# Kernel optimization log

Measured on AMD Instinct MI355X. Metric: run time of the kernel, lower is better.

The kernel has to match this reference:

```python
import jax, jax.numpy as jnp
import numpy as np

B, L, E, H, Dff = 2, 2048, 1024, 16, 4096
Dh = E // H


def _ln(x, g, b, eps=1e-5):
    m = jnp.mean(x, axis=-1, keepdims=True)
    v = jnp.mean((x - m) ** 2, axis=-1, keepdims=True)
    return (x - m) / jnp.sqrt(v + eps) * g + b


def setup_inputs() -> dict:
    key = jax.random.key(0)
    ks = jax.random.split(key, 16)
    s_e = 1.0 / np.sqrt(E)
    s_d = 1.0 / np.sqrt(Dff)
    inp = {
        "x": jax.random.normal(ks[0], (B, L, E), jnp.float32),
        # causal mask: positions with 0 are masked out (masked_fill(mask==0, -1e9))
        "mask": jnp.tril(jnp.ones((L, L), jnp.bool_)),
        # per-head QKV projections, stacked over heads: (H, E, Dh), biases (H, Dh)
        "Wq": jax.random.uniform(ks[1], (H, E, Dh), jnp.float32, -s_e, s_e),
        "bq": jax.random.uniform(ks[2], (H, Dh), jnp.float32, -s_e, s_e),
        "Wk": jax.random.uniform(ks[3], (H, E, Dh), jnp.float32, -s_e, s_e),
        "bk": jax.random.uniform(ks[4], (H, Dh), jnp.float32, -s_e, s_e),
        "Wv": jax.random.uniform(ks[5], (H, E, Dh), jnp.float32, -s_e, s_e),
        "bv": jax.random.uniform(ks[6], (H, Dh), jnp.float32, -s_e, s_e),
        "Wo": jax.random.uniform(ks[7], (E, E), jnp.float32, -s_e, s_e),
        "bo": jax.random.uniform(ks[8], (E,), jnp.float32, -s_e, s_e),
        "W1": jax.random.uniform(ks[9], (E, Dff), jnp.float32, -s_e, s_e),
        "c1": jax.random.uniform(ks[10], (Dff,), jnp.float32, -s_e, s_e),
        "W2": jax.random.uniform(ks[11], (Dff, E), jnp.float32, -s_d, s_d),
        "c2": jax.random.uniform(ks[12], (E,), jnp.float32, -s_d, s_d),
        "g1": jnp.ones((E,), jnp.float32),
        "beta1": jnp.zeros((E,), jnp.float32),
        "g2": jnp.ones((E,), jnp.float32),
        "beta2": jnp.zeros((E,), jnp.float32),
    }
    return inp


def reference(x, mask, Wq, bq, Wk, bk, Wv, bv, Wo, bo, W1, c1, W2, c2, g1, beta1, g2, beta2):
    # Batched equivalent of the per-head Attention loop (eval mode: dropout = identity)
    q = jnp.einsum("ble,hed->bhld", x, Wq) + bq[None, :, None, :]
    k = jnp.einsum("ble,hed->bhld", x, Wk) + bk[None, :, None, :]
    v = jnp.einsum("ble,hed->bhld", x, Wv) + bv[None, :, None, :]
    scores = jnp.einsum("bhld,bhmd->bhlm", q, k) / np.sqrt(Dh).astype(np.float32)
    scores = jnp.where(mask[None, None, :, :], scores, -1e9)
    p = jax.nn.softmax(scores, axis=-1)
    z = jnp.einsum("bhlm,bhmd->bhld", p, v)  # (B,H,L,Dh)
    z = z.transpose(0, 2, 1, 3).reshape(B, L, E)  # concat heads
    att = z @ Wo + bo
    h = _ln(x + att, g1, beta1)
    ff = jax.nn.relu(h @ W1 + c1) @ W2 + c2
    out = _ln(h + ff, g2, beta2)
    return out
```

## Files before the change

kernel.cpp:

```cpp
#include <hip/hip_runtime.h>
#include <hip/hip_bf16.h>
#include <math.h>

#define B_   2
#define L_   2048
#define E_   1024
#define H_   16
#define DH   64
#define DFF  4096
#define M_   4096
#define APAD 72
#define SCALE_Q 0.18033688011112042f

typedef __attribute__((ext_vector_type(8))) short short8;
typedef __attribute__((ext_vector_type(4))) float f32x4;
typedef __bf16 bf16x8 __attribute__((ext_vector_type(8)));

__device__ __forceinline__ float bf2f(unsigned short u) {
    return __uint_as_float(((unsigned)u) << 16);
}
__device__ __forceinline__ unsigned short f2bf(float f) {
    unsigned u = __float_as_uint(f);
    return (unsigned short)((u + 0x7fff + ((u >> 16) & 1)) >> 16);
}
__device__ __forceinline__ unsigned pk_trunc(float lo, float hi) {
    return (__float_as_uint(lo) >> 16) | (__float_as_uint(hi) & 0xffff0000u);
}

__device__ __forceinline__ void gld16(const unsigned short* g, unsigned short* l) {
    __builtin_amdgcn_global_load_lds(
        (const __attribute__((address_space(1))) void*)g,
        (__attribute__((address_space(3))) void*)l, 16, 0, 0);
}

__global__ __launch_bounds__(256) void prep(const float* __restrict__ x,
                                            const float* __restrict__ Wq,
                                            const float* __restrict__ Wk,
                                            const float* __restrict__ Wv,
                                            const float* __restrict__ bq,
                                            const float* __restrict__ bk,
                                            const float* __restrict__ bv,
                                            const float* __restrict__ Wo,
                                            const float* __restrict__ W1,
                                            const float* __restrict__ W2,
                                            unsigned short* __restrict__ xb,
                                            unsigned short* __restrict__ Wqkvt,
                                            unsigned short* __restrict__ Wot,
                                            unsigned short* __restrict__ W1t,
                                            unsigned short* __restrict__ W2t,
                                            float* __restrict__ bqkv) {
    __shared__ float tile[32][33];
    int bid = blockIdx.x;
    const int t = threadIdx.x;

    if (bid < 4096) {
        int i = (bid * 256 + t) * 4;
        float4 v = *(const float4*)&x[i];
        ushort4 pk = { f2bf(v.x), f2bf(v.y), f2bf(v.z), f2bf(v.w) };
        *(ushort4*)&xb[i] = pk;
        return;
    }
    bid -= 4096;

    const float* in; unsigned short* outp; int R, C, r0, c0; float sc = 1.f;
    if (bid < 3072) {
        int xq = bid & 1, yq = (bid >> 1) & 31, wh = bid >> 6;
        int which = wh >> 4, h = wh & 15;
        in   = (which == 0 ? Wq : which == 1 ? Wk : Wv) + (size_t)h * E_ * DH;
        outp = Wqkvt + ((size_t)which * 1024 + h * 64) * 1024;
        R = E_; C = DH; r0 = yq * 32; c0 = xq * 32;
        if (which == 0) sc = SCALE_Q;
    } else if (bid < 4096) {
        bid -= 3072;
        in = Wo; outp = Wot; R = E_; C = E_;
        c0 = (bid & 31) * 32; r0 = (bid >> 5) * 32;
    } else if (bid < 8192) {
        bid -= 4096;
        in = W1; outp = W1t; R = E_; C = DFF;
        c0 = (bid & 127) * 32; r0 = (bid >> 7) * 32;
    } else if (bid < 12288) {
        bid -= 8192;
        in = W2; outp = W2t; R = DFF; C = E_;
        c0 = (bid & 31) * 32; r0 = (bid >> 5) * 32;
    } else {
        bid -= 12288;
        int n = bid * 256 + t;
        bqkv[n] = n < 1024 ? bq[n] * SCALE_Q : n < 2048 ? bk[n - 1024] : bv[n - 2048];
        return;
    }

    const int tx = t & 31, tq = t >> 5;
#pragma unroll
    for (int s2 = 0; s2 < 4; s2++)
        tile[tq * 4 + s2][tx] = in[(size_t)(r0 + tq * 4 + s2) * C + c0 + tx] * sc;
    __syncthreads();
#pragma unroll
    for (int s2 = 0; s2 < 4; s2++)
        outp[(size_t)(c0 + tq * 4 + s2) * R + r0 + tx] = f2bf(tile[tx][tq * 4 + s2]);
}

__global__ __launch_bounds__(256) void v_transpose_perm(const unsigned short* __restrict__ qkv,
                                                        unsigned short* __restrict__ vtg) {
    __shared__ unsigned short tile[64 * APAD];
    const int t  = threadIdx.x;
    const int kt = blockIdx.x, hh = blockIdx.y, b = blockIdx.z;
    const int rr0 = t >> 3, o8 = (t & 7) * 8, rr1 = rr0 + 32;
    const size_t gbase = ((size_t)b * L_ + kt * 64) * 3072 + 2048 + hh * 64;
    *(short8*)&tile[rr0 * APAD + o8] = *(const short8*)&qkv[gbase + (size_t)rr0 * 3072 + o8];
    *(short8*)&tile[rr1 * APAD + o8] = *(const short8*)&qkv[gbase + (size_t)rr1 * 3072 + o8];
    __syncthreads();
    const size_t obase = ((size_t)(b * H_ + hh) * 64) * (size_t)L_ + kt * 64;
    const int a = t & 15, d0 = (t >> 4) * 4;
#pragma unroll
    for (int s2 = 0; s2 < 4; s2++) {
        int d = d0 + s2;
        ushort4 pk = { tile[(a +  0) * APAD + d], tile[(a + 16) * APAD + d],
                       tile[(a + 32) * APAD + d], tile[(a + 48) * APAD + d] };
        *(ushort4*)&vtg[obase + (size_t)d * L_ + 4 * a] = pk;
    }
}

#define BAR() __builtin_amdgcn_s_barrier()
#define LGKM0() do { asm volatile("s_waitcnt lgkmcnt(0)" ::: "memory"); \
                     __builtin_amdgcn_sched_barrier(0); } while (0)

#define G256_READ_A(qr) do {                                                  \
    _Pragma("unroll") for (int mi = 0; mi < 4; mi++)                          \
    _Pragma("unroll") for (int ks = 0; ks < 2; ks++)                          \
        afr[mi][ks] = *(const bf16x8*)&As[bb + ((qr) * 128 + aRow + mi * 16) * 64 + (ks ? cs1 : cs0)]; \
} while (0)

#define G256_READ_B(qc) do {                                                  \
    _Pragma("unroll") for (int nj = 0; nj < 2; nj++)                          \
    _Pragma("unroll") for (int ks = 0; ks < 2; ks++)                          \
        bfr[qc][nj][ks] = *(const bf16x8*)&Bs[bb + ((qc) * 128 + bRow + nj * 16) * 64 + (ks ? cs1 : cs0)]; \
} while (0)

#define G256_MFMA(qr, qc) do {                                                \
    __builtin_amdgcn_s_setprio(1);                                            \
    _Pragma("unroll") for (int mi = 0; mi < 4; mi++)                          \
    _Pragma("unroll") for (int nj = 0; nj < 2; nj++)                          \
    _Pragma("unroll") for (int ks = 0; ks < 2; ks++)                          \
        acc[qr][qc][mi][nj] = __builtin_amdgcn_mfma_f32_16x16x32_bf16(        \
            afr[mi][ks], bfr[qc][nj][ks], acc[qr][qc][mi][nj], 0, 0, 0);      \
    __builtin_amdgcn_s_setprio(0);                                            \
} while (0)

template <int RELU, int SK>
__global__ __launch_bounds__(512, 2) void gemm256(const unsigned short* __restrict__ A,
                                                  const unsigned short* __restrict__ Bt,
                                                  const float* __restrict__ bias,
                                                  unsigned short* __restrict__ P0,
                                                  unsigned short* __restrict__ P1,
                                                  unsigned short* __restrict__ P2,
                                                  unsigned short* __restrict__ P3,
                                                  int M, int N, int K) {
    extern __shared__ __align__(16) unsigned short g_lds[];
    unsigned short* As = g_lds;
    unsigned short* Bs = g_lds + 32768;

    const int t    = threadIdx.x;
    const int lane = t & 63;
    const int w    = t >> 6;
    const int quad = lane >> 4;
    const int l16  = lane & 15;

    const int lin = blockIdx.x;
    const int xcd = lin & 7, s = lin >> 3;
    const int m0 = ((xcd << 1) | (s & 1)) * 256;
    const int rest = s >> 1;
    int n0, kbeg, KT;
    unsigned short* C;
    if (SK) {
        n0 = (rest & 3) * 256;
        const int z  = rest >> 2;
        const int K4 = K >> 2;
        kbeg = z * K4;
        KT   = K4 >> 6;
        C = (z == 0) ? P0 : (z == 1) ? P1 : (z == 2) ? P2 : P3;
    } else {
        n0 = rest * 256;
        kbeg = 0;
        KT   = K >> 6;
        C = P0;
    }

    const int srow = t >> 3;
    const int ksw  = ((t & 7) ^ (srow & 7)) * 8;
    const size_t aStage = (size_t)(m0 + srow) * K + kbeg + ksw;
    const size_t bStage = (size_t)(n0 + srow) * K + kbeg + ksw;

    auto stageA = [&](int buf, int h, int v) {
        size_t g = aStage + (size_t)(h * 128) * K + (size_t)v * 64;
        unsigned short* l = As + buf * 16384 + h * 8192 + w * 512;
        gld16(A + g, l);
        gld16(A + g + (size_t)64 * K, l + 4096);
    };
    auto stageB = [&](int buf, int h, int v) {
        size_t g = bStage + (size_t)(h * 128) * K + (size_t)v * 64;
        unsigned short* l = Bs + buf * 16384 + h * 8192 + w * 512;
        gld16(Bt + g, l);
        gld16(Bt + g + (size_t)64 * K, l + 4096);
    };

    const int aRow = (w >> 2) * 64 + l16;
    const int bRow = (w & 3) * 32 + l16;
    const int cs0  = (quad ^ (l16 & 7)) * 8;
    const int cs1  = cs0 ^ 32;

    f32x4 acc[2][2][4][2];
#pragma unroll
    for (int a1 = 0; a1 < 2; a1++)
#pragma unroll
        for (int a2 = 0; a2 < 2; a2++)
#pragma unroll
            for (int a3 = 0; a3 < 4; a3++)
#pragma unroll
                for (int a4 = 0; a4 < 2; a4++)
                    acc[a1][a2][a3][a4] = (f32x4){0.f, 0.f, 0.f, 0.f};

    bf16x8 afr[4][2], bfr[2][2][2];

    stageA(0, 0, 0); stageA(0, 1, 0); stageB(0, 0, 0); stageB(0, 1, 0);
    if (KT > 1) {
        stageA(1, 0, 1); stageB(1, 0, 1);
        asm volatile("s_waitcnt vmcnt(4)" ::: "memory");
    } else {
        asm volatile("s_waitcnt vmcnt(0)" ::: "memory");
    }
    BAR();

    for (int u = 0; u < KT; ++u) {
        const int bb = (u & 1) * 16384;
        const int nb = ((u + 1) & 1);

        G256_READ_A(0);
        G256_READ_B(0);
        if (u + 1 < KT) stageB(nb, 1, u + 1);
        BAR(); LGKM0();
        G256_MFMA(0, 0);
        BAR();

        G256_READ_B(1);
        if (u + 1 < KT) stageA(nb, 1, u + 1);
        BAR(); LGKM0();
        G256_MFMA(0, 1);
        BAR();

        G256_READ_A(1);
        if (u + 2 < KT) stageA(u & 1, 0, u + 2);
        BAR(); LGKM0();
        G256_MFMA(1, 0);
        BAR();

        if (u + 2 < KT) {
            stageB(u & 1, 0, u + 2);
            asm volatile("s_waitcnt vmcnt(4)" ::: "memory");
        } else {
            asm volatile("s_waitcnt vmcnt(0)" ::: "memory");
        }
        BAR(); LGKM0();
        G256_MFMA(1, 1);
        BAR();
    }

#pragma unroll
    for (int qr = 0; qr < 2; qr++)
#pragma unroll
        for (int qc = 0; qc < 2; qc++)
#pragma unroll
            for (int nj = 0; nj < 2; nj++) {
                const int col = n0 + qc * 128 + (w & 3) * 32 + nj * 16 + l16;
                const float bv = SK ? 0.f : bias[col];
#pragma unroll
                for (int mi = 0; mi < 4; mi++) {
                    const int row = m0 + qr * 128 + (w >> 2) * 64 + mi * 16 + quad * 4;
#pragma unroll
                    for (int r = 0; r < 4; r++) {
                        float v = acc[qr][qc][mi][nj][r] + bv;
                        if (RELU) v = fmaxf(v, 0.f);
                        C[(size_t)(row + r) * N + col] = f2bf(v);
                    }
                }
            }
}

__global__ __launch_bounds__(256, 3) void attn_mfma(const unsigned short* __restrict__ qkv,
                                                    const unsigned short* __restrict__ vtg,
                                                    unsigned short* __restrict__ zb) {
    __shared__ __align__(16) unsigned short ks[2][64 * APAD];
    __shared__ __align__(16) unsigned short vt[64 * APAD];
    __shared__ __align__(16) unsigned short ps[128 * APAD];

    const int t    = threadIdx.x;
    const int lane = t & 63;
    const int w    = t >> 6;
    const int l16  = lane & 15;
    const int quad = lane >> 4;

    const int lin  = blockIdx.x;
    const int xcd  = lin & 7;
    const int s    = lin >> 3;
    const int hh   = xcd * 2 + (s & 1);
    const int rest = s >> 1;
    const int b    = rest & 1;
    const int qq0  = rest >> 1;
    const int qq   = b ? qq0 : 15 - qq0;

    const size_t rowbase = (size_t)b * L_;
    const size_t vbase   = ((size_t)(b * H_ + hh) * 64) * (size_t)L_;

    bf16x8 qf[2][2];
#pragma unroll
    for (int g = 0; g < 2; g++) {
        size_t qrow = rowbase + qq * 128 + w * 32 + g * 16 + l16;
#pragma unroll
        for (int c = 0; c < 2; c++)
            qf[g][c] = *(const bf16x8*)&qkv[qrow * 3072 + hh * 64 + c * 32 + quad * 8];
    }

    f32x4 o[2][4];
#pragma unroll
    for (int g = 0; g < 2; g++)
#pragma unroll
        for (int j = 0; j < 4; j++) o[g][j] = (f32x4){0.f, 0.f, 0.f, 0.f};
    float l_i[2][4] = {};

    const int rr0 = t >> 3, o8 = (t & 7) * 8, rr1 = rr0 + 32;
    const int ktmax = 2 * qq + 1;

    {
        size_t kg = rowbase * 3072 + 1024 + hh * 64;
        short8 k0 = *(const short8*)&qkv[kg + (size_t)rr0 * 3072 + o8];
        short8 k1 = *(const short8*)&qkv[kg + (size_t)rr1 * 3072 + o8];
        short8 v0 = *(const short8*)&vtg[vbase + (size_t)rr0 * L_ + o8];
        short8 v1 = *(const short8*)&vtg[vbase + (size_t)rr1 * L_ + o8];
        *(short8*)&ks[0][rr0 * APAD + o8] = k0;
        *(short8*)&ks[0][rr1 * APAD + o8] = k1;
        *(short8*)&vt[rr0 * APAD + o8] = v0;
        *(short8*)&vt[rr1 * APAD + o8] = v1;
    }

    short8 kr0, kr1, vr0, vr1;
    for (int kt = 0; kt <= ktmax; kt++) {
        const int p = kt & 1;
        __syncthreads();

        if (kt < ktmax) {
            size_t kg = (rowbase + (kt + 1) * 64) * 3072 + 1024 + hh * 64;
            kr0 = *(const short8*)&qkv[kg + (size_t)rr0 * 3072 + o8];
            kr1 = *(const short8*)&qkv[kg + (size_t)rr1 * 3072 + o8];
            size_t vg = vbase + (kt + 1) * 64;
            vr0 = *(const short8*)&vtg[vg + (size_t)rr0 * L_ + o8];
            vr1 = *(const short8*)&vtg[vg + (size_t)rr1 * L_ + o8];
        }

        f32x4 s4[2][4];
#pragma unroll
        for (int g = 0; g < 2; g++)
#pragma unroll
            for (int j = 0; j < 4; j++) s4[g][j] = (f32x4){0.f, 0.f, 0.f, 0.f};
#pragma unroll
        for (int c = 0; c < 2; c++)
#pragma unroll
            for (int j = 0; j < 4; j++) {
                bf16x8 kf = *(const bf16x8*)&ks[p][(j * 16 + l16) * APAD + c * 32 + quad * 8];
#pragma unroll
                for (int g = 0; g < 2; g++)
                    s4[g][j] = __builtin_amdgcn_mfma_f32_16x16x32_bf16(qf[g][c], kf, s4[g][j], 0, 0, 0);
            }

        if (kt >= 2 * qq) {
#pragma unroll
            for (int g = 0; g < 2; g++)
#pragma unroll
                for (int j = 0; j < 4; j++) {
                    int lk = kt * 64 + j * 16 + l16;
#pragma unroll
                    for (int r = 0; r < 4; r++)
                        if (lk > qq * 128 + w * 32 + g * 16 + quad * 4 + r)
                            s4[g][j][r] = -INFINITY;
                }
        }

#pragma unroll
        for (int g = 0; g < 2; g++)
#pragma unroll
            for (int r = 0; r < 4; r++) {
                float p0 = __builtin_amdgcn_exp2f(s4[g][0][r]);
                float p1 = __builtin_amdgcn_exp2f(s4[g][1][r]);
                float p2 = __builtin_amdgcn_exp2f(s4[g][2][r]);
                float p3 = __builtin_amdgcn_exp2f(s4[g][3][r]);
                l_i[g][r] += (p0 + p1) + (p2 + p3);
                uint2 pk = { pk_trunc(p0, p1), pk_trunc(p2, p3) };
                *(uint2*)&ps[(w * 32 + g * 16 + quad * 4 + r) * APAD + 4 * l16] = pk;
            }

        __builtin_amdgcn_s_waitcnt(0xc07f);

#pragma unroll
        for (int c = 0; c < 2; c++) {
            bf16x8 pf[2];
#pragma unroll
            for (int g = 0; g < 2; g++)
                pf[g] = *(const bf16x8*)&ps[(w * 32 + g * 16 + l16) * APAD + c * 32 + quad * 8];
#pragma unroll
            for (int j = 0; j < 4; j++) {
                bf16x8 vf = *(const bf16x8*)&vt[(j * 16 + l16) * APAD + c * 32 + quad * 8];
#pragma unroll
                for (int g = 0; g < 2; g++)
                    o[g][j] = __builtin_amdgcn_mfma_f32_16x16x32_bf16(pf[g], vf, o[g][j], 0, 0, 0);
            }
        }

        __syncthreads();
        if (kt < ktmax) {
            *(short8*)&ks[p ^ 1][rr0 * APAD + o8] = kr0;
            *(short8*)&ks[p ^ 1][rr1 * APAD + o8] = kr1;
            *(short8*)&vt[rr0 * APAD + o8] = vr0;
            *(short8*)&vt[rr1 * APAD + o8] = vr1;
        }
    }

#pragma unroll
    for (int g = 0; g < 2; g++)
#pragma unroll
        for (int r = 0; r < 4; r++) {
            float l = l_i[g][r];
            l += __shfl_xor(l, 1);
            l += __shfl_xor(l, 2);
            l += __shfl_xor(l, 4);
            l += __shfl_xor(l, 8);
            float inv = 1.f / l;
            size_t row = rowbase + qq * 128 + w * 32 + g * 16 + quad * 4 + r;
#pragma unroll
            for (int j = 0; j < 4; j++)
                zb[row * 1024 + hh * 64 + j * 16 + l16] = f2bf(o[g][j][r] * inv);
        }
}

template <int WRITE_BF16>
__global__ __launch_bounds__(256) void ln5_kernel(const float* __restrict__ a,
                                                  const unsigned short* __restrict__ q0,
                                                  const unsigned short* __restrict__ q1,
                                                  const unsigned short* __restrict__ q2,
                                                  const unsigned short* __restrict__ q3,
                                                  const float* __restrict__ bias,
                                                  const float* __restrict__ g,
                                                  const float* __restrict__ be,
                                                  float* __restrict__ out,
                                                  unsigned short* __restrict__ out_bf) {
    __shared__ float s1[256], s2[256];
    const int row = blockIdx.x;
    const int t   = threadIdx.x;
    const size_t base = (size_t)row * E_ + t * 4;

    float4 ya = *(const float4*)&a[base];
    ushort4 u0 = *(const ushort4*)&q0[base];
    ushort4 u1 = *(const ushort4*)&q1[base];
    ushort4 u2 = *(const ushort4*)&q2[base];
    ushort4 u3 = *(const ushort4*)&q3[base];
    float4 bb = *(const float4*)&bias[t * 4];
    float y0 = ya.x + bb.x + bf2f(u0.x) + bf2f(u1.x) + bf2f(u2.x) + bf2f(u3.x);
    float y1 = ya.y + bb.y + bf2f(u0.y) + bf2f(u1.y) + bf2f(u2.y) + bf2f(u3.y);
    float y2 = ya.z + bb.z + bf2f(u0.z) + bf2f(u1.z) + bf2f(u2.z) + bf2f(u3.z);
    float y3 = ya.w + bb.w + bf2f(u0.w) + bf2f(u1.w) + bf2f(u2.w) + bf2f(u3.w);

    s1[t] = y0 + y1 + y2 + y3;
    s2[t] = y0 * y0 + y1 * y1 + y2 * y2 + y3 * y3;
    __syncthreads();
    for (int off = 128; off > 0; off >>= 1) {
        if (t < off) { s1[t] += s1[t + off]; s2[t] += s2[t + off]; }
        __syncthreads();
    }
    float mean = s1[0] * (1.0f / E_);
    float var  = s2[0] * (1.0f / E_) - mean * mean;
    float rstd = rsqrtf(var + 1e-5f);

    float4 gv = *(const float4*)&g[t * 4];
    float4 bv = *(const float4*)&be[t * 4];
    float4 ov;
    ov.x = (y0 - mean) * rstd * gv.x + bv.x;
    ov.y = (y1 - mean) * rstd * gv.y + bv.y;
    ov.z = (y2 - mean) * rstd * gv.z + bv.z;
    ov.w = (y3 - mean) * rstd * gv.w + bv.w;
    *(float4*)&out[base] = ov;
    if (WRITE_BF16) {
        ushort4 pk = { f2bf(ov.x), f2bf(ov.y), f2bf(ov.z), f2bf(ov.w) };
        *(ushort4*)&out_bf[base] = pk;
    }
}

extern "C" void kernel_launch(void* const* d_in, const int* in_sizes, int n_in,
                              void* d_out, int out_size, void* d_ws, size_t ws_size,
                              hipStream_t stream)
{
    const float* x     = (const float*)d_in[0];
    const float* Wq    = (const float*)d_in[2];
    const float* bq    = (const float*)d_in[3];
    const float* Wk    = (const float*)d_in[4];
    const float* bk    = (const float*)d_in[5];
    const float* Wv    = (const float*)d_in[6];
    const float* bv    = (const float*)d_in[7];
    const float* Wo    = (const float*)d_in[8];
    const float* bo    = (const float*)d_in[9];
    const float* W1    = (const float*)d_in[10];
    const float* c1    = (const float*)d_in[11];
    const float* W2    = (const float*)d_in[12];
    const float* c2    = (const float*)d_in[13];
    const float* g1    = (const float*)d_in[14];
    const float* beta1 = (const float*)d_in[15];
    const float* g2    = (const float*)d_in[16];
    const float* beta2 = (const float*)d_in[17];
    float* out = (float*)d_out;

    const size_t MB = 1024 * 1024;
    char* w = (char*)d_ws;
    unsigned short* xb    = (unsigned short*)(w + 0 * MB);
    unsigned short* Wqkvt = (unsigned short*)(w + 8 * MB);
    unsigned short* Wot   = (unsigned short*)(w + 14 * MB);
    unsigned short* W1t   = (unsigned short*)(w + 16 * MB);
    unsigned short* W2t   = (unsigned short*)(w + 24 * MB);
    float*          bqkv  = (float*)(w + 32 * MB);
    unsigned short* qkv   = (unsigned short*)(w + 33 * MB);
    unsigned short* zb    = (unsigned short*)(w + 57 * MB);
    float*          h     = (float*)(w + 65 * MB);
    unsigned short* vtg   = (unsigned short*)(w + 89 * MB);
    unsigned short* ap0   = (unsigned short*)(w + 33 * MB);
    unsigned short* ap1   = (unsigned short*)(w + 41 * MB);
    unsigned short* ap2   = (unsigned short*)(w + 49 * MB);
    unsigned short* ap3   = (unsigned short*)(w + 89 * MB);
    unsigned short* hb    = (unsigned short*)(w + 0 * MB);
    unsigned short* ff1b  = (unsigned short*)(w + 33 * MB);
    unsigned short* fp0   = (unsigned short*)(w + 0 * MB);
    unsigned short* fp1   = (unsigned short*)(w + 8 * MB);
    unsigned short* fp2   = (unsigned short*)(w + 16 * MB);
    unsigned short* fp3   = (unsigned short*)(w + 81 * MB);

    static bool lds_inited = false;
    if (!lds_inited) {
        (void)hipFuncSetAttribute((const void*)&gemm256<0, 0>,
                                  hipFuncAttributeMaxDynamicSharedMemorySize, 131072);
        (void)hipFuncSetAttribute((const void*)&gemm256<1, 0>,
                                  hipFuncAttributeMaxDynamicSharedMemorySize, 131072);
        (void)hipFuncSetAttribute((const void*)&gemm256<0, 1>,
                                  hipFuncAttributeMaxDynamicSharedMemorySize, 131072);
        lds_inited = true;
    }

    dim3 blk(256);
    dim3 blk2(512);

    prep<<<dim3(16396), blk, 0, stream>>>(x, Wq, Wk, Wv, bq, bk, bv, Wo, W1, W2,
                                          xb, Wqkvt, Wot, W1t, W2t, bqkv);

    gemm256<0, 0><<<dim3(192), blk2, 131072, stream>>>(xb, Wqkvt, bqkv,
                                                       qkv, nullptr, nullptr, nullptr,
                                                       M_, 3072, E_);

    v_transpose_perm<<<dim3(L_ / 64, H_, B_), blk, 0, stream>>>(qkv, vtg);

    attn_mfma<<<dim3(512), blk, 0, stream>>>(qkv, vtg, zb);

    gemm256<0, 1><<<dim3(256), blk2, 131072, stream>>>(zb, Wot, nullptr,
                                                       ap0, ap1, ap2, ap3,
                                                       M_, E_, E_);

    ln5_kernel<1><<<dim3(M_), blk, 0, stream>>>(x, ap0, ap1, ap2, ap3, bo, g1, beta1, h, hb);

    gemm256<1, 0><<<dim3(256), blk2, 131072, stream>>>(hb, W1t, c1,
                                                       ff1b, nullptr, nullptr, nullptr,
                                                       M_, DFF, E_);

    gemm256<0, 1><<<dim3(256), blk2, 131072, stream>>>(ff1b, W2t, nullptr,
                                                       fp0, fp1, fp2, fp3,
                                                       M_, E_, DFF);

    ln5_kernel<0><<<dim3(M_), blk, 0, stream>>>(h, fp0, fp1, fp2, fp3, c2, g2, beta2, out, nullptr);
}
```

Baseline: 341.3 us.

## Split attention work across 8 waves with 16 query rows each

The attention kernel now launches 512 threads per block, and each of 8 waves owns 16 query rows instead of 4 waves owning 32 rows each. Per-wave register state (Q fragments, accumulators, row sums) is halved, and each thread loads one K and one V chunk per tile instead of two. The aim is more resident waves and better latency hiding. In exchange, each K/V fragment read from LDS is reused for half as many MFMAs, so LDS traffic per FLOP doubles, and block-wide barriers now have to synchronize twice as many waves.

```diff
diff --git a/kernel.cpp b/kernel.cpp
--- a/kernel.cpp
+++ b/kernel.cpp
@@ -285,7 +285,7 @@
             }
 }
 
-__global__ __launch_bounds__(256, 3) void attn_mfma(const unsigned short* __restrict__ qkv,
+__global__ __launch_bounds__(512, 4) void attn_mfma(const unsigned short* __restrict__ qkv,
                                                     const unsigned short* __restrict__ vtg,
                                                     unsigned short* __restrict__ zb) {
     __shared__ __align__(16) unsigned short ks[2][64 * APAD];
@@ -310,133 +310,106 @@
     const size_t rowbase = (size_t)b * L_;
     const size_t vbase   = ((size_t)(b * H_ + hh) * 64) * (size_t)L_;
 
-    bf16x8 qf[2][2];
-#pragma unroll
-    for (int g = 0; g < 2; g++) {
-        size_t qrow = rowbase + qq * 128 + w * 32 + g * 16 + l16;
+    bf16x8 qf[2];
+    {
+        size_t qrow = rowbase + qq * 128 + w * 16 + l16;
 #pragma unroll
         for (int c = 0; c < 2; c++)
-            qf[g][c] = *(const bf16x8*)&qkv[qrow * 3072 + hh * 64 + c * 32 + quad * 8];
-    }
-
-    f32x4 o[2][4];
-#pragma unroll
-    for (int g = 0; g < 2; g++)
-#pragma unroll
-        for (int j = 0; j < 4; j++) o[g][j] = (f32x4){0.f, 0.f, 0.f, 0.f};
-    float l_i[2][4] = {};
-
-    const int rr0 = t >> 3, o8 = (t & 7) * 8, rr1 = rr0 + 32;
+            qf[c] = *(const bf16x8*)&qkv[qrow * 3072 + hh * 64 + c * 32 + quad * 8];
+    }
+
+    f32x4 o[4];
+#pragma unroll
+    for (int j = 0; j < 4; j++) o[j] = (f32x4){0.f, 0.f, 0.f, 0.f};
+    float l_i[4] = {};
+
+    const int rr = t >> 3, o8 = (t & 7) * 8;
     const int ktmax = 2 * qq + 1;
 
     {
         size_t kg = rowbase * 3072 + 1024 + hh * 64;
-        short8 k0 = *(const short8*)&qkv[kg + (size_t)rr0 * 3072 + o8];
-        short8 k1 = *(const short8*)&qkv[kg + (size_t)rr1 * 3072 + o8];
-        short8 v0 = *(const short8*)&vtg[vbase + (size_t)rr0 * L_ + o8];
-        short8 v1 = *(const short8*)&vtg[vbase + (size_t)rr1 * L_ + o8];
-        *(short8*)&ks[0][rr0 * APAD + o8] = k0;
-        *(short8*)&ks[0][rr1 * APAD + o8] = k1;
-        *(short8*)&vt[rr0 * APAD + o8] = v0;
-        *(short8*)&vt[rr1 * APAD + o8] = v1;
-    }
-
-    short8 kr0, kr1, vr0, vr1;
+        short8 k0 = *(const short8*)&qkv[kg + (size_t)rr * 3072 + o8];
+        short8 v0 = *(const short8*)&vtg[vbase + (size_t)rr * L_ + o8];
+        *(short8*)&ks[0][rr * APAD + o8] = k0;
+        *(short8*)&vt[rr * APAD + o8] = v0;
+    }
+
+    short8 kr0, vr0;
     for (int kt = 0; kt <= ktmax; kt++) {
         const int p = kt & 1;
         __syncthreads();
 
         if (kt < ktmax) {
             size_t kg = (rowbase + (kt + 1) * 64) * 3072 + 1024 + hh * 64;
-            kr0 = *(const short8*)&qkv[kg + (size_t)rr0 * 3072 + o8];
-            kr1 = *(const short8*)&qkv[kg + (size_t)rr1 * 3072 + o8];
-            size_t vg = vbase + (kt + 1) * 64;
-            vr0 = *(const short8*)&vtg[vg + (size_t)rr0 * L_ + o8];
-            vr1 = *(const short8*)&vtg[vg + (size_t)rr1 * L_ + o8];
+            kr0 = *(const short8*)&qkv[kg + (size_t)rr * 3072 + o8];
+            vr0 = *(const short8*)&vtg[vbase + (kt + 1) * 64 + (size_t)rr * L_ + o8];
         }
 
-        f32x4 s4[2][4];
-#pragma unroll
-        for (int g = 0; g < 2; g++)
-#pragma unroll
-            for (int j = 0; j < 4; j++) s4[g][j] = (f32x4){0.f, 0.f, 0.f, 0.f};
+        f32x4 s4[4];
+#pragma unroll
+        for (int j = 0; j < 4; j++) s4[j] = (f32x4){0.f, 0.f, 0.f, 0.f};
 #pragma unroll
         for (int c = 0; c < 2; c++)
 #pragma unroll
             for (int j = 0; j < 4; j++) {
                 bf16x8 kf = *(const bf16x8*)&ks[p][(j * 16 + l16) * APAD + c * 32 + quad * 8];
-#pragma unroll
-                for (int g = 0; g < 2; g++)
-                    s4[g][j] = __builtin_amdgcn_mfma_f32_16x16x32_bf16(qf[g][c], kf, s4[g][j], 0, 0, 0);
+                s4[j] = __builtin_amdgcn_mfma_f32_16x16x32_bf16(qf[c], kf, s4[j], 0, 0, 0);
             }
 
         if (kt >= 2 * qq) {
 #pragma unroll
-            for (int g = 0; g < 2; g++)
-#pragma unroll
-                for (int j = 0; j < 4; j++) {
-                    int lk = kt * 64 + j * 16 + l16;
-#pragma unroll
-                    for (int r = 0; r < 4; r++)
-                        if (lk > qq * 128 + w * 32 + g * 16 + quad * 4 + r)
-                            s4[g][j][r] = -INFINITY;
-                }
+            for (int j = 0; j < 4; j++) {
+                int lk = kt * 64 + j * 16 + l16;
+#pragma unroll
+                for (int r = 0; r < 4; r++)
+                    if (lk > qq * 128 + w * 16 + quad * 4 + r)
+                        s4[j][r] = -INFINITY;
+            }
         }
 
 #pragma unroll
-        for (int g = 0; g < 2; g++)
-#pragma unroll
-            for (int r = 0; r < 4; r++) {
-                float p0 = __builtin_amdgcn_exp2f(s4[g][0][r]);
-                float p1 = __builtin_amdgcn_exp2f(s4[g][1][r]);
-                float p2 = __builtin_amdgcn_exp2f(s4[g][2][r]);
-                float p3 = __builtin_amdgcn_exp2f(s4[g][3][r]);
-                l_i[g][r] += (p0 + p1) + (p2 + p3);
-                uint2 pk = { pk_trunc(p0, p1), pk_trunc(p2, p3) };
-                *(uint2*)&ps[(w * 32 + g * 16 + quad * 4 + r) * APAD + 4 * l16] = pk;
-            }
+        for (int r = 0; r < 4; r++) {
+            float p0 = __builtin_amdgcn_exp2f(s4[0][r]);
+            float p1 = __builtin_amdgcn_exp2f(s4[1][r]);
+            float p2 = __builtin_amdgcn_exp2f(s4[2][r]);
+            float p3 = __builtin_amdgcn_exp2f(s4[3][r]);
+            l_i[r] += (p0 + p1) + (p2 + p3);
+            uint2 pk = { pk_trunc(p0, p1), pk_trunc(p2, p3) };
+            *(uint2*)&ps[(w * 16 + quad * 4 + r) * APAD + 4 * l16] = pk;
+        }
 
         __builtin_amdgcn_s_waitcnt(0xc07f);
 
 #pragma unroll
         for (int c = 0; c < 2; c++) {
-            bf16x8 pf[2];
-#pragma unroll
-            for (int g = 0; g < 2; g++)
-                pf[g] = *(const bf16x8*)&ps[(w * 32 + g * 16 + l16) * APAD + c * 32 + quad * 8];
+            bf16x8 pf = *(const bf16x8*)&ps[(w * 16 + l16) * APAD + c * 32 + quad * 8];
 #pragma unroll
             for (int j = 0; j < 4; j++) {
                 bf16x8 vf = *(const bf16x8*)&vt[(j * 16 + l16) * APAD + c * 32 + quad * 8];
-#pragma unroll
-                for (int g = 0; g < 2; g++)
-                    o[g][j] = __builtin_amdgcn_mfma_f32_16x16x32_bf16(pf[g], vf, o[g][j], 0, 0, 0);
+                o[j] = __builtin_amdgcn_mfma_f32_16x16x32_bf16(pf, vf, o[j], 0, 0, 0);
             }
         }
 
         __syncthreads();
         if (kt < ktmax) {
-            *(short8*)&ks[p ^ 1][rr0 * APAD + o8] = kr0;
-            *(short8*)&ks[p ^ 1][rr1 * APAD + o8] = kr1;
-            *(short8*)&vt[rr0 * APAD + o8] = vr0;
-            *(short8*)&vt[rr1 * APAD + o8] = vr1;
+            *(short8*)&ks[p ^ 1][rr * APAD + o8] = kr0;
+            *(short8*)&vt[rr * APAD + o8] = vr0;
         }
     }
 
 #pragma unroll
-    for (int g = 0; g < 2; g++)
-#pragma unroll
-        for (int r = 0; r < 4; r++) {
-            float l = l_i[g][r];
-            l += __shfl_xor(l, 1);
-            l += __shfl_xor(l, 2);
-            l += __shfl_xor(l, 4);
-            l += __shfl_xor(l, 8);
-            float inv = 1.f / l;
-            size_t row = rowbase + qq * 128 + w * 32 + g * 16 + quad * 4 + r;
-#pragma unroll
-            for (int j = 0; j < 4; j++)
-                zb[row * 1024 + hh * 64 + j * 16 + l16] = f2bf(o[g][j][r] * inv);
-        }
+    for (int r = 0; r < 4; r++) {
+        float l = l_i[r];
+        l += __shfl_xor(l, 1);
+        l += __shfl_xor(l, 2);
+        l += __shfl_xor(l, 4);
+        l += __shfl_xor(l, 8);
+        float inv = 1.f / l;
+        size_t row = rowbase + qq * 128 + w * 16 + quad * 4 + r;
+#pragma unroll
+        for (int j = 0; j < 4; j++)
+            zb[row * 1024 + hh * 64 + j * 16 + l16] = f2bf(o[j][r] * inv);
+    }
 }
 
 template <int WRITE_BF16>
@@ -560,7 +533,7 @@
 
     v_transpose_perm<<<dim3(L_ / 64, H_, B_), blk, 0, stream>>>(qkv, vtg);
 
-    attn_mfma<<<dim3(512), blk, 0, stream>>>(qkv, vtg, zb);
+    attn_mfma<<<dim3(512), blk2, 0, stream>>>(qkv, vtg, zb);
 
     gemm256<0, 1><<<dim3(256), blk2, 131072, stream>>>(zb, Wot, nullptr,
                                                        ap0, ap1, ap2, ap3,
```

Result: no change. 338.2 us (-0.9%).

## Split attention KV range across two blocks with paired q-tiles and combine pass

Applied to the files above, without the earlier changes.

Each attention block now processes a pair of query tiles (qq and 15-qq) and only even or odd KV tiles, based on a new unit index. This balances causal work across blocks. Partial fp32 outputs and row sums go to workspace, and a new attn_combine kernel sums the halves, normalises and writes bf16 z. The MFMA sections also gain s_setprio hints and launch bounds drop to 2 blocks per CU. In exchange, the extra kernel launch and the fp32 partial traffic add cost.

```diff
diff --git a/kernel.cpp b/kernel.cpp
--- a/kernel.cpp
+++ b/kernel.cpp
@@ -285,9 +285,12 @@
             }
 }
 
-__global__ __launch_bounds__(256, 3) void attn_mfma(const unsigned short* __restrict__ qkv,
+__global__ __launch_bounds__(256, 2) void attn_mfma(const unsigned short* __restrict__ qkv,
                                                     const unsigned short* __restrict__ vtg,
-                                                    unsigned short* __restrict__ zb) {
+                                                    float* __restrict__ oA,
+                                                    float* __restrict__ oB,
+                                                    float* __restrict__ lA,
+                                                    float* __restrict__ lB) {
     __shared__ __align__(16) unsigned short ks[2][64 * APAD];
     __shared__ __align__(16) unsigned short vt[64 * APAD];
     __shared__ __align__(16) unsigned short ps[128 * APAD];
@@ -299,144 +302,180 @@
     const int quad = lane >> 4;
 
     const int lin  = blockIdx.x;
-    const int xcd  = lin & 7;
-    const int s    = lin >> 3;
+    const int unit = lin >> 8;
+    const int l8   = lin & 255;
+    const int xcd  = l8 & 7;
+    const int s    = l8 >> 3;
     const int hh   = xcd * 2 + (s & 1);
     const int rest = s >> 1;
     const int b    = rest & 1;
-    const int qq0  = rest >> 1;
-    const int qq   = b ? qq0 : 15 - qq0;
+    const int pair = rest >> 1;
+
+    float* __restrict__ oP = unit ? oB : oA;
+    float* __restrict__ lP = unit ? lB : lA;
 
     const size_t rowbase = (size_t)b * L_;
     const size_t vbase   = ((size_t)(b * H_ + hh) * 64) * (size_t)L_;
-
-    bf16x8 qf[2][2];
-#pragma unroll
-    for (int g = 0; g < 2; g++) {
-        size_t qrow = rowbase + qq * 128 + w * 32 + g * 16 + l16;
-#pragma unroll
-        for (int c = 0; c < 2; c++)
-            qf[g][c] = *(const bf16x8*)&qkv[qrow * 3072 + hh * 64 + c * 32 + quad * 8];
-    }
-
-    f32x4 o[2][4];
-#pragma unroll
-    for (int g = 0; g < 2; g++)
-#pragma unroll
-        for (int j = 0; j < 4; j++) o[g][j] = (f32x4){0.f, 0.f, 0.f, 0.f};
-    float l_i[2][4] = {};
-
     const int rr0 = t >> 3, o8 = (t & 7) * 8, rr1 = rr0 + 32;
-    const int ktmax = 2 * qq + 1;
-
-    {
-        size_t kg = rowbase * 3072 + 1024 + hh * 64;
-        short8 k0 = *(const short8*)&qkv[kg + (size_t)rr0 * 3072 + o8];
-        short8 k1 = *(const short8*)&qkv[kg + (size_t)rr1 * 3072 + o8];
-        short8 v0 = *(const short8*)&vtg[vbase + (size_t)rr0 * L_ + o8];
-        short8 v1 = *(const short8*)&vtg[vbase + (size_t)rr1 * L_ + o8];
-        *(short8*)&ks[0][rr0 * APAD + o8] = k0;
-        *(short8*)&ks[0][rr1 * APAD + o8] = k1;
-        *(short8*)&vt[rr0 * APAD + o8] = v0;
-        *(short8*)&vt[rr1 * APAD + o8] = v1;
-    }
-
-    short8 kr0, kr1, vr0, vr1;
-    for (int kt = 0; kt <= ktmax; kt++) {
-        const int p = kt & 1;
-        __syncthreads();
-
-        if (kt < ktmax) {
-            size_t kg = (rowbase + (kt + 1) * 64) * 3072 + 1024 + hh * 64;
-            kr0 = *(const short8*)&qkv[kg + (size_t)rr0 * 3072 + o8];
-            kr1 = *(const short8*)&qkv[kg + (size_t)rr1 * 3072 + o8];
-            size_t vg = vbase + (kt + 1) * 64;
-            vr0 = *(const short8*)&vtg[vg + (size_t)rr0 * L_ + o8];
-            vr1 = *(const short8*)&vtg[vg + (size_t)rr1 * L_ + o8];
+
+    for (int ph = 0; ph < 2; ph++) {
+        const int qq = ph ? pair : 15 - pair;
+        const int cnt = qq + 1;
+
+        bf16x8 qf[2][2];
+#pragma unroll
+        for (int g = 0; g < 2; g++) {
+            size_t qrow = rowbase + qq * 128 + w * 32 + g * 16 + l16;
+#pragma unroll
+            for (int c = 0; c < 2; c++)
+                qf[g][c] = *(const bf16x8*)&qkv[qrow * 3072 + hh * 64 + c * 32 + quad * 8];
         }
 
-        f32x4 s4[2][4];
+        f32x4 o[2][4];
 #pragma unroll
         for (int g = 0; g < 2; g++)
 #pragma unroll
-            for (int j = 0; j < 4; j++) s4[g][j] = (f32x4){0.f, 0.f, 0.f, 0.f};
-#pragma unroll
-        for (int c = 0; c < 2; c++)
-#pragma unroll
-            for (int j = 0; j < 4; j++) {
-                bf16x8 kf = *(const bf16x8*)&ks[p][(j * 16 + l16) * APAD + c * 32 + quad * 8];
+            for (int j = 0; j < 4; j++) o[g][j] = (f32x4){0.f, 0.f, 0.f, 0.f};
+        float l_i[2][4] = {};
+
+        {
+            size_t kg = (rowbase + unit * 64) * 3072 + 1024 + hh * 64;
+            short8 k0 = *(const short8*)&qkv[kg + (size_t)rr0 * 3072 + o8];
+            short8 k1 = *(const short8*)&qkv[kg + (size_t)rr1 * 3072 + o8];
+            short8 v0 = *(const short8*)&vtg[vbase + unit * 64 + (size_t)rr0 * L_ + o8];
+            short8 v1 = *(const short8*)&vtg[vbase + unit * 64 + (size_t)rr1 * L_ + o8];
+            *(short8*)&ks[0][rr0 * APAD + o8] = k0;
+            *(short8*)&ks[0][rr1 * APAD + o8] = k1;
+            *(short8*)&vt[rr0 * APAD + o8] = v0;
+            *(short8*)&vt[rr1 * APAD + o8] = v1;
+        }
+
+        short8 kr0, kr1, vr0, vr1;
+        for (int i = 0; i < cnt; i++) {
+            const int kt = unit + 2 * i;
+            const int p  = i & 1;
+            __syncthreads();
+
+            if (i + 1 < cnt) {
+                size_t kg = (rowbase + (kt + 2) * 64) * 3072 + 1024 + hh * 64;
+                kr0 = *(const short8*)&qkv[kg + (size_t)rr0 * 3072 + o8];
+                kr1 = *(const short8*)&qkv[kg + (size_t)rr1 * 3072 + o8];
+                size_t vg = vbase + (kt + 2) * 64;
+                vr0 = *(const short8*)&vtg[vg + (size_t)rr0 * L_ + o8];
+                vr1 = *(const short8*)&vtg[vg + (size_t)rr1 * L_ + o8];
+            }
+
+            f32x4 s4[2][4];
+#pragma unroll
+            for (int g = 0; g < 2; g++)
+#pragma unroll
+                for (int j = 0; j < 4; j++) s4[g][j] = (f32x4){0.f, 0.f, 0.f, 0.f};
+            __builtin_amdgcn_s_setprio(1);
+#pragma unroll
+            for (int c = 0; c < 2; c++)
+#pragma unroll
+                for (int j = 0; j < 4; j++) {
+                    bf16x8 kf = *(const bf16x8*)&ks[p][(j * 16 + l16) * APAD + c * 32 + quad * 8];
+#pragma unroll
+                    for (int g = 0; g < 2; g++)
+                        s4[g][j] = __builtin_amdgcn_mfma_f32_16x16x32_bf16(qf[g][c], kf, s4[g][j], 0, 0, 0);
+                }
+            __builtin_amdgcn_s_setprio(0);
+
+            if (kt >= 2 * qq) {
 #pragma unroll
                 for (int g = 0; g < 2; g++)
-                    s4[g][j] = __builtin_amdgcn_mfma_f32_16x16x32_bf16(qf[g][c], kf, s4[g][j], 0, 0, 0);
+#pragma unroll
+                    for (int j = 0; j < 4; j++) {
+                        int lk = kt * 64 + j * 16 + l16;
+#pragma unroll
+                        for (int r = 0; r < 4; r++)
+                            if (lk > qq * 128 + w * 32 + g * 16 + quad * 4 + r)
+                                s4[g][j][r] = -INFINITY;
+                    }
             }
 
-        if (kt >= 2 * qq) {
 #pragma unroll
             for (int g = 0; g < 2; g++)
 #pragma unroll
+                for (int r = 0; r < 4; r++) {
+                    float p0 = __builtin_amdgcn_exp2f(s4[g][0][r]);
+                    float p1 = __builtin_amdgcn_exp2f(s4[g][1][r]);
+                    float p2 = __builtin_amdgcn_exp2f(s4[g][2][r]);
+                    float p3 = __builtin_amdgcn_exp2f(s4[g][3][r]);
+                    l_i[g][r] += (p0 + p1) + (p2 + p3);
+                    uint2 pk = { pk_trunc(p0, p1), pk_trunc(p2, p3) };
+                    *(uint2*)&ps[(w * 32 + g * 16 + quad * 4 + r) * APAD + 4 * l16] = pk;
+                }
+
+            __builtin_amdgcn_s_waitcnt(0xc07f);
+
+            __builtin_amdgcn_s_setprio(1);
+#pragma unroll
+            for (int c = 0; c < 2; c++) {
+                bf16x8 pf[2];
+#pragma unroll
+                for (int g = 0; g < 2; g++)
+                    pf[g] = *(const bf16x8*)&ps[(w * 32 + g * 16 + l16) * APAD + c * 32 + quad * 8];
+#pragma unroll
                 for (int j = 0; j < 4; j++) {
-                    int lk = kt * 64 + j * 16 + l16;
-#pragma unroll
-                    for (int r = 0; r < 4; r++)
-                        if (lk > qq * 128 + w * 32 + g * 16 + quad * 4 + r)
-                            s4[g][j][r] = -INFINITY;
+                    bf16x8 vf = *(const bf16x8*)&vt[(j * 16 + l16) * APAD + c * 32 + quad * 8];
+#pragma unroll
+                    for (int g = 0; g < 2; g++)
+                        o[g][j] = __builtin_amdgcn_mfma_f32_16x16x32_bf16(pf[g], vf, o[g][j], 0, 0, 0);
                 }
-        }
-
-#pragma unroll
-        for (int g = 0; g < 2; g++)
-#pragma unroll
-            for (int r = 0; r < 4; r++) {
-                float p0 = __builtin_amdgcn_exp2f(s4[g][0][r]);
-                float p1 = __builtin_amdgcn_exp2f(s4[g][1][r]);
-                float p2 = __builtin_amdgcn_exp2f(s4[g][2][r]);
-                float p3 = __builtin_amdgcn_exp2f(s4[g][3][r]);
-                l_i[g][r] += (p0 + p1) + (p2 + p3);
-                uint2 pk = { pk_trunc(p0, p1), pk_trunc(p2, p3) };
-                *(uint2*)&ps[(w * 32 + g * 16 + quad * 4 + r) * APAD + 4 * l16] = pk;
             }
-
-        __builtin_amdgcn_s_waitcnt(0xc07f);
-
-#pragma unroll
-        for (int c = 0; c < 2; c++) {
-            bf16x8 pf[2];
-#pragma unroll
-            for (int g = 0; g < 2; g++)
-                pf[g] = *(const bf16x8*)&ps[(w * 32 + g * 16 + l16) * APAD + c * 32 + quad * 8];
-#pragma unroll
-            for (int j = 0; j < 4; j++) {
-                bf16x8 vf = *(const bf16x8*)&vt[(j * 16 + l16) * APAD + c * 32 + quad * 8];
-#pragma unroll
-                for (int g = 0; g < 2; g++)
-                    o[g][j] = __builtin_amdgcn_mfma_f32_16x16x32_bf16(pf[g], vf, o[g][j], 0, 0, 0);
+            __builtin_amdgcn_s_setprio(0);
+
+            __syncthreads();
+            if (i + 1 < cnt) {
+                *(short8*)&ks[p ^ 1][rr0 * APAD + o8] = kr0;
+                *(short8*)&ks[p ^ 1][rr1 * APAD + o8] = kr1;
+                *(short8*)&vt[rr0 * APAD + o8] = vr0;
+                *(short8*)&vt[rr1 * APAD + o8] = vr1;
             }
         }
 
-        __syncthreads();
-        if (kt < ktmax) {
-            *(short8*)&ks[p ^ 1][rr0 * APAD + o8] = kr0;
-            *(short8*)&ks[p ^ 1][rr1 * APAD + o8] = kr1;
-            *(short8*)&vt[rr0 * APAD + o8] = vr0;
-            *(short8*)&vt[rr1 * APAD + o8] = vr1;
-        }
-    }
-
-#pragma unroll
-    for (int g = 0; g < 2; g++)
-#pragma unroll
-        for (int r = 0; r < 4; r++) {
-            float l = l_i[g][r];
-            l += __shfl_xor(l, 1);
-            l += __shfl_xor(l, 2);
-            l += __shfl_xor(l, 4);
-            l += __shfl_xor(l, 8);
-            float inv = 1.f / l;
-            size_t row = rowbase + qq * 128 + w * 32 + g * 16 + quad * 4 + r;
-#pragma unroll
-            for (int j = 0; j < 4; j++)
-                zb[row * 1024 + hh * 64 + j * 16 + l16] = f2bf(o[g][j][r] * inv);
-        }
+#pragma unroll
+        for (int g = 0; g < 2; g++)
+#pragma unroll
+            for (int r = 0; r < 4; r++) {
+                float l = l_i[g][r];
+                l += __shfl_xor(l, 1);
+                l += __shfl_xor(l, 2);
+                l += __shfl_xor(l, 4);
+                l += __shfl_xor(l, 8);
+                int rowq = qq * 128 + w * 32 + g * 16 + quad * 4 + r;
+                size_t grow = (size_t)(b * H_ + hh) * L_ + rowq;
+                if (l16 == 0) lP[grow] = l;
+#pragma unroll
+                for (int j = 0; j < 4; j++)
+                    oP[grow * 64 + j * 16 + l16] = o[g][j][r];
+            }
+    }
+}
+
+__global__ __launch_bounds__(256) void attn_combine(const float* __restrict__ oA,
+                                                    const float* __restrict__ oB,
+                                                    const float* __restrict__ lA,
+                                                    const float* __restrict__ lB,
+                                                    unsigned short* __restrict__ zb) {
+    const int t = threadIdx.x;
+    const size_t idx4 = ((size_t)blockIdx.x * 256 + t) * 4;
+    const size_t row  = idx4 >> 6;
+    const int    col  = (int)(idx4 & 63);
+
+    float inv = 1.f / (lA[row] + lB[row]);
+    float4 a = *(const float4*)&oA[idx4];
+    float4 c = *(const float4*)&oB[idx4];
+
+    const int bq   = (int)(row >> 15);
+    const int hh   = (int)((row >> 11) & 15);
+    const int rowq = (int)(row & 2047);
+    size_t z = ((size_t)(bq * L_ + rowq)) * 1024 + hh * 64 + col;
+    ushort4 pk = { f2bf((a.x + c.x) * inv), f2bf((a.y + c.y) * inv),
+                   f2bf((a.z + c.z) * inv), f2bf((a.w + c.w) * inv) };
+    *(ushort4*)&zb[z] = pk;
 }
 
 template <int WRITE_BF16>
@@ -523,9 +562,13 @@
     unsigned short* W2t   = (unsigned short*)(w + 24 * MB);
     float*          bqkv  = (float*)(w + 32 * MB);
     unsigned short* qkv   = (unsigned short*)(w + 33 * MB);
-    unsigned short* zb    = (unsigned short*)(w + 57 * MB);
     float*          h     = (float*)(w + 65 * MB);
     unsigned short* vtg   = (unsigned short*)(w + 89 * MB);
+    float*          oPA   = (float*)(w + 57 * MB);
+    float*          oPB   = (float*)(w + 73 * MB);
+    float*          lPA   = (float*)(w + 32 * MB);
+    float*          lPB   = (float*)(w + 32 * MB + 262144);
+    unsigned short* zb    = (unsigned short*)(w + 0 * MB);
     unsigned short* ap0   = (unsigned short*)(w + 33 * MB);
     unsigned short* ap1   = (unsigned short*)(w + 41 * MB);
     unsigned short* ap2   = (unsigned short*)(w + 49 * MB);
@@ -560,7 +603,9 @@
 
     v_transpose_perm<<<dim3(L_ / 64, H_, B_), blk, 0, stream>>>(qkv, vtg);
 
-    attn_mfma<<<dim3(512), blk, 0, stream>>>(qkv, vtg, zb);
+    attn_mfma<<<dim3(512), blk, 0, stream>>>(qkv, vtg, oPA, oPB, lPA, lPB);
+
+    attn_combine<<<dim3(4096), blk, 0, stream>>>(oPA, oPB, lPA, lPB, zb);
 
     gemm256<0, 1><<<dim3(256), blk2, 131072, stream>>>(zb, Wot, nullptr,
                                                        ap0, ap1, ap2, ap3,
```

Measured after the change: 335.6 us. No clear change (-1.6%).
